# Kernel optimization log

Hardware: AMD Instinct MI355X
Metric: run time of the kernel (lower is better)

The kernel has to match this reference:

```python
import jax, jax.numpy as jnp
import numpy as np

# Irreps structure: (multiplicity, component dim 2l+1) for 64x0e + 32x1o + 16x2e
MULTS = (64, 32, 16)
DIMS = (1, 3, 5)
N_NODES = 65536
NUM_TYPES = 64


def setup_inputs() -> dict:
    key = jax.random.key(0)
    k_x, k_idx, k0, k1, k2 = jax.random.split(key, 5)
    dim = sum(m * d for m, d in zip(MULTS, DIMS))  # 240
    x = jax.random.normal(k_x, (N_NODES, dim), dtype=jnp.float32)
    idx = jax.random.randint(k_idx, (N_NODES,), 0, NUM_TYPES)
    W0 = jax.random.normal(k0, (NUM_TYPES, 64, 64), dtype=jnp.float32)
    W1 = jax.random.normal(k1, (NUM_TYPES, 32, 32), dtype=jnp.float32)
    W2 = jax.random.normal(k2, (NUM_TYPES, 16, 16), dtype=jnp.float32)
    return {"x": x, "W0": W0, "W1": W1, "W2": W2, "idx": idx}


def reference(x, W0, W1, W2, idx):
    """Indexed e3nn-style linear: per-node index gathers a weight set; each
    irrep block mixes multiplicity channels (shared across the 2l+1 components)
    with e3nn path normalization 1/sqrt(m_in)."""
    n = x.shape[0]
    outs = []
    off = 0
    for W, m, d in zip((W0, W1, W2), MULTS, DIMS):
        blk = x[:, off:off + m * d].reshape(n, m, d)  # [N, m_in, 2l+1]
        off += m * d
        Wn = W[idx]  # gather per-node weights: [N, m_in, m_out]
        scale = np.float32(1.0 / np.sqrt(m))
        out = jnp.einsum('nio,nid->nod', Wn, blk) * scale  # [N, m_out, 2l+1]
        outs.append(out.reshape(n, m * d))
    return jnp.concatenate(outs, axis=-1)
```

## Files before the change

### kernel.cpp

```cpp
#include <hip/hip_runtime.h>

typedef __attribute__((ext_vector_type(8))) short short8;
typedef __attribute__((ext_vector_type(4))) float floatx4;
typedef __attribute__((ext_vector_type(4))) unsigned uintx4;

#define NTYPES    64
#define WT_STRIDE 5632
#define WROWS     16
#define CPAD      16

__device__ __forceinline__ unsigned short f2bf(float f) {
    union { float f; unsigned u; } v; v.f = f;
    unsigned u = v.u;
    u += 0x7FFFu + ((u >> 16) & 1u);
    return (unsigned short)(u >> 16);
}

__device__ __forceinline__ unsigned pk2(float lo, float hi) {
    unsigned r;
    asm("v_cvt_pk_bf16_f32 %0, %1, %2" : "=v"(r) : "v"(lo), "v"(hi));
    return r;
}

__global__ __launch_bounds__(256) void wt_kernel(const float* __restrict__ W0,
                                                 const float* __restrict__ W1,
                                                 const float* __restrict__ W2,
                                                 unsigned short* __restrict__ wt,
                                                 int* __restrict__ gcount) {
    __shared__ float ws0[4096];
    __shared__ float ws1[1024];
    __shared__ float ws2[256];
    const int t = blockIdx.x, tid = threadIdx.x;
    if (t == 0 && tid < NTYPES) gcount[tid * CPAD] = 0;
    const float4* s0 = (const float4*)(W0 + (size_t)t * 4096);
#pragma unroll
    for (int j = 0; j < 4; ++j) ((float4*)ws0)[j * 256 + tid] = s0[j * 256 + tid];
    ((float4*)ws1)[tid] = ((const float4*)(W1 + (size_t)t * 1024))[tid];
    if (tid < 64) ((float4*)ws2)[tid] = ((const float4*)(W2 + (size_t)t * 256))[tid];
    __syncthreads();
    unsigned short* dst = wt + (size_t)t * WT_STRIDE;
    for (int e = tid; e < 4096; e += 256) {
        int f = e >> 9, rem = e & 511, rr = rem >> 5, k2 = rem & 31;
        int i = (f & 1) * 32 + k2, o = (f >> 1) * 16 + rr;
        dst[e] = f2bf(ws0[i * 64 + o] * 0.125f);
    }
    for (int e = tid; e < 1024; e += 256) {
        int h = e >> 9, rem = e & 511, rr = rem >> 5, k = rem & 31;
        dst[4096 + e] = f2bf(ws1[k * 32 + h * 16 + rr] * 0.17677669529663687f);
    }
    for (int e = tid; e < 512; e += 256) {
        int rr = e >> 5, k = e & 31;
        dst[5120 + e] = (k < 16) ? f2bf(ws2[k * 16 + rr] * 0.25f) : (unsigned short)0;
    }
}

__global__ __launch_bounds__(256) void hist_kernel(const int* __restrict__ idx,
                                                   int* __restrict__ gcount, int n) {
    __shared__ int c[NTYPES];
    const int tid = threadIdx.x, g = blockIdx.x * 256 + tid;
    if (tid < NTYPES) c[tid] = 0;
    __syncthreads();
    if (g < n) atomicAdd(&c[idx[g]], 1);
    __syncthreads();
    if (tid < NTYPES && c[tid]) atomicAdd(&gcount[tid * CPAD], c[tid]);
}

__global__ __launch_bounds__(64) void base_kernel(const int* __restrict__ gcount,
                                                  int* __restrict__ gcur) {
    const int t = threadIdx.x;
    int v = gcount[t * CPAD];
    int s = v;
#pragma unroll
    for (int o = 1; o < 64; o <<= 1) {
        int u = __shfl_up(s, o);
        if (t >= o) s += u;
    }
    gcur[t * CPAD] = s - v;
}

__global__ __launch_bounds__(256) void scatter_kernel(const int* __restrict__ idx,
                                                      int* __restrict__ gcur,
                                                      int* __restrict__ psort, int n) {
    __shared__ int c[NTYPES], off[NTYPES], cur[NTYPES];
    const int tid = threadIdx.x, g = blockIdx.x * 256 + tid;
    if (tid < NTYPES) { c[tid] = 0; cur[tid] = 0; }
    __syncthreads();
    int ty = -1;
    if (g < n) { ty = idx[g]; atomicAdd(&c[ty], 1); }
    __syncthreads();
    if (tid < NTYPES && c[tid]) off[tid] = atomicAdd(&gcur[tid * CPAD], c[tid]);
    __syncthreads();
    if (g < n) {
        int rk = atomicAdd(&cur[ty], 1);
        psort[off[ty] + rk] = g | (ty << 24);
    }
}

__global__ __launch_bounds__(256, 4) void main_kernel(
    const float* __restrict__ x,
    const int* __restrict__ psort,
    const unsigned short* __restrict__ wt,
    float* __restrict__ out, int n)
{
    const int tid = threadIdx.x, wv = tid >> 6, ln = tid & 63;
    const int w = blockIdx.x * 4 + wv;
    const int nbase = w * WROWS;
    if (nbase >= n) return;
    const int nv = min(WROWS, n - nbase);

    int pl = 0;
    if (ln < WROWS && (nbase + ln) < n) pl = psort[nbase + ln];

    const int r = ln & 15, q4 = ln >> 4;
    const int prow = __shfl(pl, min(r, nv - 1));
    const int node = prow & 0xFFFFFF;
    const float* xp = x + (size_t)node * 240;

    union frag { short8 s; uintx4 u; };

    float4 f0a = *(const float4*)(xp + q4 * 8);
    float4 f0b = *(const float4*)(xp + q4 * 8 + 4);
    float4 f0c = *(const float4*)(xp + 32 + q4 * 8);
    float4 f0d = *(const float4*)(xp + 32 + q4 * 8 + 4);
    frag bx0, bx1;
    bx0.u = uintx4{pk2(f0a.x, f0a.y), pk2(f0a.z, f0a.w),
                   pk2(f0b.x, f0b.y), pk2(f0b.z, f0b.w)};
    bx1.u = uintx4{pk2(f0c.x, f0c.y), pk2(f0c.z, f0c.w),
                   pk2(f0d.x, f0d.y), pk2(f0d.z, f0d.w)};

    const float4* xg = (const float4*)(xp + 64 + q4 * 24);
    float4 g0 = xg[0], g1 = xg[1], g2 = xg[2], g3 = xg[3], g4 = xg[4], g5 = xg[5];
    const float G[24] = {g0.x, g0.y, g0.z, g0.w, g1.x, g1.y, g1.z, g1.w,
                         g2.x, g2.y, g2.z, g2.w, g3.x, g3.y, g3.z, g3.w,
                         g4.x, g4.y, g4.z, g4.w, g5.x, g5.y, g5.z, g5.w};
    frag b1d[3];
#pragma unroll
    for (int d = 0; d < 3; ++d)
        b1d[d].u = uintx4{pk2(G[d], G[3 + d]), pk2(G[6 + d], G[9 + d]),
                          pk2(G[12 + d], G[15 + d]), pk2(G[18 + d], G[21 + d])};

    const float4* xh = (const float4*)(xp + 160 + (q4 & 1) * 40);
    float4 h0 = xh[0], h1 = xh[1], h2 = xh[2], h3 = xh[3], h4 = xh[4];
    float4 h5 = xh[5], h6 = xh[6], h7 = xh[7], h8 = xh[8], h9 = xh[9];
    const float H[40] = {h0.x, h0.y, h0.z, h0.w, h1.x, h1.y, h1.z, h1.w,
                         h2.x, h2.y, h2.z, h2.w, h3.x, h3.y, h3.z, h3.w,
                         h4.x, h4.y, h4.z, h4.w, h5.x, h5.y, h5.z, h5.w,
                         h6.x, h6.y, h6.z, h6.w, h7.x, h7.y, h7.z, h7.w,
                         h8.x, h8.y, h8.z, h8.w, h9.x, h9.y, h9.z, h9.w};
    frag b2d[5];
#pragma unroll
    for (int d = 0; d < 5; ++d)
        b2d[d].u = uintx4{pk2(H[d], H[5 + d]), pk2(H[10 + d], H[15 + d]),
                          pk2(H[20 + d], H[25 + d]), pk2(H[30 + d], H[35 + d])};

    const bool vrow = (r < nv);
    float* op = out + (size_t)node * 240;

    int ti  = __shfl(pl, r) >> 24;
    int tim = __shfl(pl, (r > 0) ? (r - 1) : 0) >> 24;
    bool bnd = (r == 0) || (ti != tim);
    unsigned m = (unsigned)(__ballot(bnd) & 0xFFFFull);

    while (m) {
        const int slo = __builtin_ctz(m);
        const unsigned m2 = m & (m - 1u);
        const int shi = m2 ? __builtin_ctz(m2) : nv;
        const int tyseg = __shfl(pl, slo) >> 24;
        const unsigned short* wb = wt + (size_t)tyseg * WT_STRIDE;
        const bool vst = vrow && (r >= slo) && (r < shi);

#pragma unroll
        for (int nt = 0; nt < 4; ++nt) {
            short8 wa = *(const short8*)(wb + (nt * 2) * 512 + r * 32 + q4 * 8);
            short8 wc = *(const short8*)(wb + (nt * 2 + 1) * 512 + r * 32 + q4 * 8);
            floatx4 ac = {0.f, 0.f, 0.f, 0.f};
            ac = __builtin_amdgcn_mfma_f32_16x16x32_bf16(wa, bx0.s, ac, 0, 0, 0);
            ac = __builtin_amdgcn_mfma_f32_16x16x32_bf16(wc, bx1.s, ac, 0, 0, 0);
            if (vst) *(floatx4*)(op + nt * 16 + q4 * 4) = ac;
        }

        {
            short8 wc0 = *(const short8*)(wb + 4096 + r * 32 + q4 * 8);
            short8 wc1 = *(const short8*)(wb + 4096 + 512 + r * 32 + q4 * 8);
            floatx4 a1[2][3];
#pragma unroll
            for (int d = 0; d < 3; ++d) {
                floatx4 z = {0.f, 0.f, 0.f, 0.f};
                a1[0][d] = __builtin_amdgcn_mfma_f32_16x16x32_bf16(wc0, b1d[d].s, z, 0, 0, 0);
                a1[1][d] = __builtin_amdgcn_mfma_f32_16x16x32_bf16(wc1, b1d[d].s, z, 0, 0, 0);
            }
            if (vst) {
#pragma unroll
                for (int h = 0; h < 2; ++h) {
                    float* o1 = op + 64 + (h * 16 + q4 * 4) * 3;
                    floatx4 v0 = {a1[h][0][0], a1[h][1][0], a1[h][2][0], a1[h][0][1]};
                    floatx4 v1 = {a1[h][1][1], a1[h][2][1], a1[h][0][2], a1[h][1][2]};
                    floatx4 v2 = {a1[h][2][2], a1[h][0][3], a1[h][1][3], a1[h][2][3]};
                    *(floatx4*)(o1)     = v0;
                    *(floatx4*)(o1 + 4) = v1;
                    *(floatx4*)(o1 + 8) = v2;
                }
            }
        }

        {
            short8 wc2 = *(const short8*)(wb + 5120 + r * 32 + q4 * 8);
            floatx4 a2[5];
#pragma unroll
            for (int d = 0; d < 5; ++d) {
                floatx4 z = {0.f, 0.f, 0.f, 0.f};
                a2[d] = __builtin_amdgcn_mfma_f32_16x16x32_bf16(wc2, b2d[d].s, z, 0, 0, 0);
            }
            if (vst) {
                float* o2 = op + 160 + q4 * 20;
                floatx4 v0 = {a2[0][0], a2[1][0], a2[2][0], a2[3][0]};
                floatx4 v1 = {a2[4][0], a2[0][1], a2[1][1], a2[2][1]};
                floatx4 v2 = {a2[3][1], a2[4][1], a2[0][2], a2[1][2]};
                floatx4 v3 = {a2[2][2], a2[3][2], a2[4][2], a2[0][3]};
                floatx4 v4 = {a2[1][3], a2[2][3], a2[3][3], a2[4][3]};
                *(floatx4*)(o2)      = v0;
                *(floatx4*)(o2 + 4)  = v1;
                *(floatx4*)(o2 + 8)  = v2;
                *(floatx4*)(o2 + 12) = v3;
                *(floatx4*)(o2 + 16) = v4;
            }
        }
        m = m2;
    }
}

extern "C" void kernel_launch(void* const* d_in, const int* in_sizes, int n_in,
                              void* d_out, int out_size, void* d_ws, size_t ws_size,
                              hipStream_t stream) {
    const float* x  = (const float*)d_in[0];
    const float* W0 = (const float*)d_in[1];
    const float* W1 = (const float*)d_in[2];
    const float* W2 = (const float*)d_in[3];
    const int*   idx = (const int*)d_in[4];
    float* out = (float*)d_out;
    const int n = in_sizes[4];
    const int nb = (n + 255) / 256;

    char* ws = (char*)d_ws;
    unsigned short* wt = (unsigned short*)ws;
    size_t off = (size_t)NTYPES * WT_STRIDE * 2;
    int* psort  = (int*)(ws + off); off += (size_t)n * 4;
    int* gcount = (int*)(ws + off); off += (size_t)NTYPES * CPAD * 4;
    int* gcur   = (int*)(ws + off);

    wt_kernel     <<<NTYPES, 256, 0, stream>>>(W0, W1, W2, wt, gcount);
    hist_kernel   <<<nb, 256, 0, stream>>>(idx, gcount, n);
    base_kernel   <<<1, 64, 0, stream>>>(gcount, gcur);
    scatter_kernel<<<nb, 256, 0, stream>>>(idx, gcur, psort, n);
    main_kernel   <<<(n + 4 * WROWS - 1) / (4 * WROWS), 256, 0, stream>>>(x, psort, wt, out, n);
}
```

Before: 150.7 us.

## Fuse histogram into weight prep and prefetch weight fragments ahead of MFMA loop

The separate histogram kernel is removed. Each weight-prep block now builds a per-block type histogram over a slice of idx, and base_kernel sums these partials before the scan, saving one launch and the global atomics. In the main kernel, all x loads and the first segment's weight fragments are issued up front behind a sched_barrier, and the next segment's weights are prefetched at the end of each loop iteration. Launch bounds drop from 4 to 3 waves per SIMD to leave room for the extra live registers, at the cost of lower occupancy.

Result: no change. 149.9 us (-0.5%).

```diff
diff --git a/kernel.cpp b/kernel.cpp
--- a/kernel.cpp
+++ b/kernel.cpp
@@ -25,19 +25,26 @@
 __global__ __launch_bounds__(256) void wt_kernel(const float* __restrict__ W0,
                                                  const float* __restrict__ W1,
                                                  const float* __restrict__ W2,
+                                                 const int* __restrict__ idx,
                                                  unsigned short* __restrict__ wt,
-                                                 int* __restrict__ gcount) {
+                                                 int* __restrict__ bh, int n) {
     __shared__ float ws0[4096];
     __shared__ float ws1[1024];
     __shared__ float ws2[256];
+    __shared__ int hc[NTYPES];
     const int t = blockIdx.x, tid = threadIdx.x;
-    if (t == 0 && tid < NTYPES) gcount[tid * CPAD] = 0;
+    if (tid < NTYPES) hc[tid] = 0;
     const float4* s0 = (const float4*)(W0 + (size_t)t * 4096);
 #pragma unroll
     for (int j = 0; j < 4; ++j) ((float4*)ws0)[j * 256 + tid] = s0[j * 256 + tid];
     ((float4*)ws1)[tid] = ((const float4*)(W1 + (size_t)t * 1024))[tid];
     if (tid < 64) ((float4*)ws2)[tid] = ((const float4*)(W2 + (size_t)t * 256))[tid];
     __syncthreads();
+    const int per = (n + NTYPES - 1) / NTYPES;
+    for (int e = tid; e < per; e += 256) {
+        int g = t * per + e;
+        if (g < n) atomicAdd(&hc[idx[g]], 1);
+    }
     unsigned short* dst = wt + (size_t)t * WT_STRIDE;
     for (int e = tid; e < 4096; e += 256) {
         int f = e >> 9, rem = e & 511, rr = rem >> 5, k2 = rem & 31;
@@ -52,23 +59,16 @@
         int rr = e >> 5, k = e & 31;
         dst[5120 + e] = (k < 16) ? f2bf(ws2[k * 16 + rr] * 0.25f) : (unsigned short)0;
     }
-}
-
-__global__ __launch_bounds__(256) void hist_kernel(const int* __restrict__ idx,
-                                                   int* __restrict__ gcount, int n) {
-    __shared__ int c[NTYPES];
-    const int tid = threadIdx.x, g = blockIdx.x * 256 + tid;
-    if (tid < NTYPES) c[tid] = 0;
-    __syncthreads();
-    if (g < n) atomicAdd(&c[idx[g]], 1);
-    __syncthreads();
-    if (tid < NTYPES && c[tid]) atomicAdd(&gcount[tid * CPAD], c[tid]);
-}
-
-__global__ __launch_bounds__(64) void base_kernel(const int* __restrict__ gcount,
+    __syncthreads();
+    if (tid < NTYPES) bh[t * NTYPES + tid] = hc[tid];
+}
+
+__global__ __launch_bounds__(64) void base_kernel(const int* __restrict__ bh,
                                                   int* __restrict__ gcur) {
     const int t = threadIdx.x;
-    int v = gcount[t * CPAD];
+    int v = 0;
+#pragma unroll
+    for (int b = 0; b < NTYPES; ++b) v += bh[b * NTYPES + t];
     int s = v;
 #pragma unroll
     for (int o = 1; o < 64; o <<= 1) {
@@ -96,7 +96,22 @@
     }
 }
 
-__global__ __launch_bounds__(256, 4) void main_kernel(
+#define LOAD_FRAGS(WB) do {                                         \
+    const unsigned short* _wp = (WB) + r * 32 + q4 * 8;             \
+    wa0 = *(const short8*)(_wp);                                    \
+    wa1 = *(const short8*)(_wp + 512);                              \
+    wa2 = *(const short8*)(_wp + 1024);                             \
+    wa3 = *(const short8*)(_wp + 1536);                             \
+    wa4 = *(const short8*)(_wp + 2048);                             \
+    wa5 = *(const short8*)(_wp + 2560);                             \
+    wa6 = *(const short8*)(_wp + 3072);                             \
+    wa7 = *(const short8*)(_wp + 3584);                             \
+    wc0 = *(const short8*)(_wp + 4096);                             \
+    wc1 = *(const short8*)(_wp + 4608);                             \
+    wc2 = *(const short8*)(_wp + 5120);                             \
+} while (0)
+
+__global__ __launch_bounds__(256, 3) void main_kernel(
     const float* __restrict__ x,
     const int* __restrict__ psort,
     const unsigned short* __restrict__ wt,
@@ -116,20 +131,32 @@
     const int node = prow & 0xFFFFFF;
     const float* xp = x + (size_t)node * 240;
 
-    union frag { short8 s; uintx4 u; };
+    int ti  = __shfl(pl, r) >> 24;
+    int tim = __shfl(pl, (r > 0) ? (r - 1) : 0) >> 24;
+    bool bnd = (r == 0) || (ti != tim);
+    unsigned m = (unsigned)(__ballot(bnd) & 0xFFFFull);
+    const int ty0 = __shfl(pl, 0) >> 24;
 
     float4 f0a = *(const float4*)(xp + q4 * 8);
     float4 f0b = *(const float4*)(xp + q4 * 8 + 4);
     float4 f0c = *(const float4*)(xp + 32 + q4 * 8);
     float4 f0d = *(const float4*)(xp + 32 + q4 * 8 + 4);
+    const float4* xg = (const float4*)(xp + 64 + q4 * 24);
+    float4 g0 = xg[0], g1 = xg[1], g2 = xg[2], g3 = xg[3], g4 = xg[4], g5 = xg[5];
+    const float4* xh = (const float4*)(xp + 160 + (q4 & 1) * 40);
+    float4 h0 = xh[0], h1 = xh[1], h2 = xh[2], h3 = xh[3], h4 = xh[4];
+    float4 h5 = xh[5], h6 = xh[6], h7 = xh[7], h8 = xh[8], h9 = xh[9];
+    short8 wa0, wa1, wa2, wa3, wa4, wa5, wa6, wa7, wc0, wc1, wc2;
+    LOAD_FRAGS(wt + (size_t)ty0 * WT_STRIDE);
+    __builtin_amdgcn_sched_barrier(0);
+
+    union frag { short8 s; uintx4 u; };
+
     frag bx0, bx1;
     bx0.u = uintx4{pk2(f0a.x, f0a.y), pk2(f0a.z, f0a.w),
                    pk2(f0b.x, f0b.y), pk2(f0b.z, f0b.w)};
     bx1.u = uintx4{pk2(f0c.x, f0c.y), pk2(f0c.z, f0c.w),
                    pk2(f0d.x, f0d.y), pk2(f0d.z, f0d.w)};
-
-    const float4* xg = (const float4*)(xp + 64 + q4 * 24);
-    float4 g0 = xg[0], g1 = xg[1], g2 = xg[2], g3 = xg[3], g4 = xg[4], g5 = xg[5];
     const float G[24] = {g0.x, g0.y, g0.z, g0.w, g1.x, g1.y, g1.z, g1.w,
                          g2.x, g2.y, g2.z, g2.w, g3.x, g3.y, g3.z, g3.w,
                          g4.x, g4.y, g4.z, g4.w, g5.x, g5.y, g5.z, g5.w};
@@ -138,10 +165,6 @@
     for (int d = 0; d < 3; ++d)
         b1d[d].u = uintx4{pk2(G[d], G[3 + d]), pk2(G[6 + d], G[9 + d]),
                           pk2(G[12 + d], G[15 + d]), pk2(G[18 + d], G[21 + d])};
-
-    const float4* xh = (const float4*)(xp + 160 + (q4 & 1) * 40);
-    float4 h0 = xh[0], h1 = xh[1], h2 = xh[2], h3 = xh[3], h4 = xh[4];
-    float4 h5 = xh[5], h6 = xh[6], h7 = xh[7], h8 = xh[8], h9 = xh[9];
     const float H[40] = {h0.x, h0.y, h0.z, h0.w, h1.x, h1.y, h1.z, h1.w,
                          h2.x, h2.y, h2.z, h2.w, h3.x, h3.y, h3.z, h3.w,
                          h4.x, h4.y, h4.z, h4.w, h5.x, h5.y, h5.z, h5.w,
@@ -156,32 +179,33 @@
     const bool vrow = (r < nv);
     float* op = out + (size_t)node * 240;
 
-    int ti  = __shfl(pl, r) >> 24;
-    int tim = __shfl(pl, (r > 0) ? (r - 1) : 0) >> 24;
-    bool bnd = (r == 0) || (ti != tim);
-    unsigned m = (unsigned)(__ballot(bnd) & 0xFFFFull);
-
-    while (m) {
+    while (true) {
         const int slo = __builtin_ctz(m);
         const unsigned m2 = m & (m - 1u);
         const int shi = m2 ? __builtin_ctz(m2) : nv;
-        const int tyseg = __shfl(pl, slo) >> 24;
-        const unsigned short* wb = wt + (size_t)tyseg * WT_STRIDE;
         const bool vst = vrow && (r >= slo) && (r < shi);
 
-#pragma unroll
-        for (int nt = 0; nt < 4; ++nt) {
-            short8 wa = *(const short8*)(wb + (nt * 2) * 512 + r * 32 + q4 * 8);
-            short8 wc = *(const short8*)(wb + (nt * 2 + 1) * 512 + r * 32 + q4 * 8);
-            floatx4 ac = {0.f, 0.f, 0.f, 0.f};
-            ac = __builtin_amdgcn_mfma_f32_16x16x32_bf16(wa, bx0.s, ac, 0, 0, 0);
-            ac = __builtin_amdgcn_mfma_f32_16x16x32_bf16(wc, bx1.s, ac, 0, 0, 0);
-            if (vst) *(floatx4*)(op + nt * 16 + q4 * 4) = ac;
+        {
+            floatx4 ac;
+            ac = floatx4{0.f, 0.f, 0.f, 0.f};
+            ac = __builtin_amdgcn_mfma_f32_16x16x32_bf16(wa0, bx0.s, ac, 0, 0, 0);
+            ac = __builtin_amdgcn_mfma_f32_16x16x32_bf16(wa1, bx1.s, ac, 0, 0, 0);
+            if (vst) *(floatx4*)(op + q4 * 4) = ac;
+            ac = floatx4{0.f, 0.f, 0.f, 0.f};
+            ac = __builtin_amdgcn_mfma_f32_16x16x32_bf16(wa2, bx0.s, ac, 0, 0, 0);
+            ac = __builtin_amdgcn_mfma_f32_16x16x32_bf16(wa3, bx1.s, ac, 0, 0, 0);
+            if (vst) *(floatx4*)(op + 16 + q4 * 4) = ac;
+            ac = floatx4{0.f, 0.f, 0.f, 0.f};
+            ac = __builtin_amdgcn_mfma_f32_16x16x32_bf16(wa4, bx0.s, ac, 0, 0, 0);
+            ac = __builtin_amdgcn_mfma_f32_16x16x32_bf16(wa5, bx1.s, ac, 0, 0, 0);
+            if (vst) *(floatx4*)(op + 32 + q4 * 4) = ac;
+            ac = floatx4{0.f, 0.f, 0.f, 0.f};
+            ac = __builtin_amdgcn_mfma_f32_16x16x32_bf16(wa6, bx0.s, ac, 0, 0, 0);
+            ac = __builtin_amdgcn_mfma_f32_16x16x32_bf16(wa7, bx1.s, ac, 0, 0, 0);
+            if (vst) *(floatx4*)(op + 48 + q4 * 4) = ac;
         }
 
         {
-            short8 wc0 = *(const short8*)(wb + 4096 + r * 32 + q4 * 8);
-            short8 wc1 = *(const short8*)(wb + 4096 + 512 + r * 32 + q4 * 8);
             floatx4 a1[2][3];
 #pragma unroll
             for (int d = 0; d < 3; ++d) {
@@ -204,7 +228,6 @@
         }
 
         {
-            short8 wc2 = *(const short8*)(wb + 5120 + r * 32 + q4 * 8);
             floatx4 a2[5];
 #pragma unroll
             for (int d = 0; d < 5; ++d) {
@@ -225,7 +248,11 @@
                 *(floatx4*)(o2 + 16) = v4;
             }
         }
+
         m = m2;
+        if (!m) break;
+        const int tyn = __shfl(pl, __builtin_ctz(m)) >> 24;
+        LOAD_FRAGS(wt + (size_t)tyn * WT_STRIDE);
     }
 }
 
@@ -244,13 +271,12 @@
     char* ws = (char*)d_ws;
     unsigned short* wt = (unsigned short*)ws;
     size_t off = (size_t)NTYPES * WT_STRIDE * 2;
-    int* psort  = (int*)(ws + off); off += (size_t)n * 4;
-    int* gcount = (int*)(ws + off); off += (size_t)NTYPES * CPAD * 4;
-    int* gcur   = (int*)(ws + off);
-
-    wt_kernel     <<<NTYPES, 256, 0, stream>>>(W0, W1, W2, wt, gcount);
-    hist_kernel   <<<nb, 256, 0, stream>>>(idx, gcount, n);
-    base_kernel   <<<1, 64, 0, stream>>>(gcount, gcur);
+    int* psort = (int*)(ws + off); off += (size_t)n * 4;
+    int* bh    = (int*)(ws + off); off += (size_t)NTYPES * NTYPES * 4;
+    int* gcur  = (int*)(ws + off);
+
+    wt_kernel     <<<NTYPES, 256, 0, stream>>>(W0, W1, W2, idx, wt, bh, n);
+    base_kernel   <<<1, 64, 0, stream>>>(bh, gcur);
     scatter_kernel<<<nb, 256, 0, stream>>>(idx, gcur, psort, n);
     main_kernel   <<<(n + 4 * WROWS - 1) / (4 * WROWS), 256, 0, stream>>>(x, psort, wt, out, n);
 }
```
